# Kernel optimization log

Hardware: AMD Instinct MI355X
Metric: run time of the kernel (lower is better)

The kernel has to match this reference:

```python
import jax, jax.numpy as jnp
import numpy as np


def _cdist(a, b, p):
    # a: [B, N, D], b: [B, M, D] -> [B, N, M] pairwise Lp distance
    diff = jnp.abs(a[:, :, None, :] - b[:, None, :, :])  # [B, N, M, D]
    if p == 1:
        return jnp.sum(diff, axis=-1)
    return jnp.sum(diff ** p, axis=-1) ** (1.0 / p)


def setup_inputs() -> dict:
    key = jax.random.key(0)
    k1, k2, k3 = jax.random.split(key, 3)
    B, P, D = 32, 2048, 2
    pred = jax.random.normal(k1, (B, P, D), dtype=jnp.float32)
    gt = jax.random.normal(k2, (B, P, D), dtype=jnp.float32)
    gt_valid = jax.random.normal(k3, (B, P, D), dtype=jnp.float32)
    return {"pred": pred, "gt": gt, "gt_valid": gt_valid, "loss_type": 1}


def reference(pred, gt, gt_valid, loss_type):
    # matrix = cdist(pred, gt): [B, Np, Ng]; torch.min(dim=1) reduces over Np
    m1 = _cdist(pred, gt, loss_type)
    pred2gt_min = jnp.min(m1, axis=1)  # [B, Ng]
    # matrix = cdist(gt_valid, pred): [B, Ngv, Np]; min over dim=1 (Ngv)
    m2 = _cdist(gt_valid, pred, loss_type)
    gt2pred_min = jnp.min(m2, axis=1)  # [B, Np]
    return jnp.mean(jnp.stack([jnp.mean(pred2gt_min), jnp.mean(gt2pred_min)]))
```

## Files before the change

### kernel.cpp

```cpp
#include <hip/hip_runtime.h>


typedef float v2f __attribute__((ext_vector_type(2)));

#define BB 32
#define NN 2048
#define TPB 512
#define WAVES 8
#define TGT 256
#define CH (NN / WAVES)
#define NTILES (NN / TGT)
#define NBLK (2 * BB * NTILES)

__global__ __launch_bounds__(TPB) void chamfer_l1_part(
    const float* __restrict__ pred,
    const float* __restrict__ gt,
    const float* __restrict__ gt_valid,
    float* __restrict__ bsum)
{
    const int bid  = blockIdx.x;
    const int dir  = bid >> 8;
    const int rem  = bid & 255;
    const int b    = rem >> 3;
    const int tile = rem & (NTILES - 1);
    const int lane = threadIdx.x & 63;
    const int wid  = threadIdx.x >> 6;

    const float* __restrict__ tgt = (dir == 0 ? gt   : pred)     + (size_t)b * NN * 2;
    const float* __restrict__ src = (dir == 0 ? pred : gt_valid) + (size_t)b * NN * 2;

    __shared__ v2f lds_src[NN];
    {
        const float4* gsrc = reinterpret_cast<const float4*>(src);
        float4*       lsrc = reinterpret_cast<float4*>(lds_src);
        lsrc[threadIdx.x]       = gsrc[threadIdx.x];
        lsrc[threadIdx.x + TPB] = gsrc[threadIdx.x + TPB];
    }

    const int j0 = tile * TGT + lane;
    v2f p0, p1, p2, p3;
    {
        float2 t0 = reinterpret_cast<const float2*>(tgt)[j0];
        float2 t1 = reinterpret_cast<const float2*>(tgt)[j0 + 64];
        float2 t2 = reinterpret_cast<const float2*>(tgt)[j0 + 128];
        float2 t3 = reinterpret_cast<const float2*>(tgt)[j0 + 192];
        p0 = (v2f){t0.x, t0.y};
        p1 = (v2f){t1.x, t1.y};
        p2 = (v2f){t2.x, t2.y};
        p3 = (v2f){t3.x, t3.y};
    }
    __syncthreads();

    const float4* __restrict__ ls4 =
        reinterpret_cast<const float4*>(lds_src + (size_t)wid * CH);

    float c00 = 1e30f, c01 = 1e30f, c10 = 1e30f, c11 = 1e30f;
    float c20 = 1e30f, c21 = 1e30f, c30 = 1e30f, c31 = 1e30f;

    #pragma unroll 2
    for (int s = 0; s < CH / 2; s += 4) {
        float4 f0 = ls4[s + 0];
        float4 f1 = ls4[s + 1];
        float4 f2 = ls4[s + 2];
        float4 f3 = ls4[s + 3];
        v2f q0 = (v2f){f0.x, f0.y}, q1 = (v2f){f0.z, f0.w};
        v2f q2 = (v2f){f1.x, f1.y}, q3 = (v2f){f1.z, f1.w};
        v2f q4 = (v2f){f2.x, f2.y}, q5 = (v2f){f2.z, f2.w};
        v2f q6 = (v2f){f3.x, f3.y}, q7 = (v2f){f3.z, f3.w};

        #define L1S(q, p) (fabsf((q).x - (p).x) + fabsf((q).y - (p).y))
        c00 = fminf(c00, fminf(L1S(q0,p0), L1S(q1,p0)));
        c00 = fminf(c00, fminf(L1S(q2,p0), L1S(q3,p0)));
        c01 = fminf(c01, fminf(L1S(q4,p0), L1S(q5,p0)));
        c01 = fminf(c01, fminf(L1S(q6,p0), L1S(q7,p0)));
        c10 = fminf(c10, fminf(L1S(q0,p1), L1S(q1,p1)));
        c10 = fminf(c10, fminf(L1S(q2,p1), L1S(q3,p1)));
        c11 = fminf(c11, fminf(L1S(q4,p1), L1S(q5,p1)));
        c11 = fminf(c11, fminf(L1S(q6,p1), L1S(q7,p1)));
        c20 = fminf(c20, fminf(L1S(q0,p2), L1S(q1,p2)));
        c20 = fminf(c20, fminf(L1S(q2,p2), L1S(q3,p2)));
        c21 = fminf(c21, fminf(L1S(q4,p2), L1S(q5,p2)));
        c21 = fminf(c21, fminf(L1S(q6,p2), L1S(q7,p2)));
        c30 = fminf(c30, fminf(L1S(q0,p3), L1S(q1,p3)));
        c30 = fminf(c30, fminf(L1S(q2,p3), L1S(q3,p3)));
        c31 = fminf(c31, fminf(L1S(q4,p3), L1S(q5,p3)));
        c31 = fminf(c31, fminf(L1S(q6,p3), L1S(q7,p3)));
        #undef L1S
    }
    const float m0 = fminf(c00, c01);
    const float m1 = fminf(c10, c11);
    const float m2 = fminf(c20, c21);
    const float m3 = fminf(c30, c31);

    __shared__ float part[WAVES][TGT];
    part[wid][lane]       = m0;
    part[wid][lane + 64]  = m1;
    part[wid][lane + 128] = m2;
    part[wid][lane + 192] = m3;
    __syncthreads();

    __shared__ float wpart[4];
    if (threadIdx.x < TGT) {
        const int t = threadIdx.x;
        float mm = part[0][t];
        #pragma unroll
        for (int w = 1; w < WAVES; ++w) mm = fminf(mm, part[w][t]);
        for (int off = 32; off > 0; off >>= 1)
            mm += __shfl_down(mm, off, 64);
        if ((t & 63) == 0) wpart[t >> 6] = mm;
    }
    __syncthreads();
    if (threadIdx.x == 0)
        bsum[bid] = (wpart[0] + wpart[1]) + (wpart[2] + wpart[3]);
}

__global__ __launch_bounds__(256) void chamfer_l1_reduce(
    const float* __restrict__ bsum,
    float* __restrict__ out)
{
    const int t = threadIdx.x;
    float2 v = reinterpret_cast<const float2*>(bsum)[t];
    float s = v.x + v.y;
    for (int off = 32; off > 0; off >>= 1)
        s += __shfl_down(s, off, 64);
    __shared__ float w[4];
    if ((t & 63) == 0) w[t >> 6] = s;
    __syncthreads();
    if (t == 0)
        out[0] = (w[0] + w[1] + w[2] + w[3]) * (1.0f / (2.0f * BB * NN));
}

extern "C" void kernel_launch(void* const* d_in, const int* in_sizes, int n_in,
                              void* d_out, int out_size, void* d_ws, size_t ws_size,
                              hipStream_t stream) {
    const float* pred     = (const float*)d_in[0];
    const float* gt       = (const float*)d_in[1];
    const float* gt_valid = (const float*)d_in[2];
    float* out  = (float*)d_out;
    float* bsum = (float*)d_ws;

    chamfer_l1_part<<<NBLK, TPB, 0, stream>>>(pred, gt, gt_valid, bsum);
    chamfer_l1_reduce<<<1, 256, 0, stream>>>(bsum, out);
}
```

Baseline: 82.08 us.

## Rotate points to compute L1 distance as Chebyshev max with packed ops

Uses the identity |dx|+|dy| = max(|du|,|dv|) with u=x+y, v=x-y. Source points are stored pre-rotated in LDS and targets are stored negated, so each pair of distances costs two packed adds, two abs-max ops and one min3 via inline asm. This roughly halves the VALU instruction count per distance in the inner loop. The rotation changes floating-point rounding slightly, and the inline asm limits compiler scheduling.

```diff
diff --git a/kernel.cpp b/kernel.cpp
--- a/kernel.cpp
+++ b/kernel.cpp
@@ -11,6 +11,22 @@
 #define CH (NN / WAVES)
 #define NTILES (NN / TGT)
 #define NBLK (2 * BB * NTILES)
+
+__device__ __forceinline__ v2f pk_add(v2f a, v2f b) {
+    v2f d;
+    asm("v_pk_add_f32 %0, %1, %2" : "=v"(d) : "v"(a), "v"(b));
+    return d;
+}
+__device__ __forceinline__ float max_abs(float a, float b) {
+    float d;
+    asm("v_max_f32 %0, abs(%1), abs(%2)" : "=v"(d) : "v"(a), "v"(b));
+    return d;
+}
+__device__ __forceinline__ float min3(float a, float b, float c) {
+    float d;
+    asm("v_min3_f32 %0, %1, %2, %3" : "=v"(d) : "v"(a), "v"(b), "v"(c));
+    return d;
+}
 
 __global__ __launch_bounds__(TPB) void chamfer_l1_part(
     const float* __restrict__ pred,
@@ -29,33 +45,39 @@
     const float* __restrict__ tgt = (dir == 0 ? gt   : pred)     + (size_t)b * NN * 2;
     const float* __restrict__ src = (dir == 0 ? pred : gt_valid) + (size_t)b * NN * 2;
 
-    __shared__ v2f lds_src[NN];
+    __shared__ float4 lds_src[NN / 2];
     {
         const float4* gsrc = reinterpret_cast<const float4*>(src);
-        float4*       lsrc = reinterpret_cast<float4*>(lds_src);
-        lsrc[threadIdx.x]       = gsrc[threadIdx.x];
-        lsrc[threadIdx.x + TPB] = gsrc[threadIdx.x + TPB];
+        float4 t0 = gsrc[threadIdx.x];
+        float4 t1 = gsrc[threadIdx.x + TPB];
+        lds_src[threadIdx.x]       = (float4){t0.x + t0.y, t0.z + t0.w,
+                                              t0.x - t0.y, t0.z - t0.w};
+        lds_src[threadIdx.x + TPB] = (float4){t1.x + t1.y, t1.z + t1.w,
+                                              t1.x - t1.y, t1.z - t1.w};
     }
 
     const int j0 = tile * TGT + lane;
-    v2f p0, p1, p2, p3;
+    v2f nu0, nv0, nu1, nv1, nu2, nv2, nu3, nv3;
     {
         float2 t0 = reinterpret_cast<const float2*>(tgt)[j0];
         float2 t1 = reinterpret_cast<const float2*>(tgt)[j0 + 64];
         float2 t2 = reinterpret_cast<const float2*>(tgt)[j0 + 128];
         float2 t3 = reinterpret_cast<const float2*>(tgt)[j0 + 192];
-        p0 = (v2f){t0.x, t0.y};
-        p1 = (v2f){t1.x, t1.y};
-        p2 = (v2f){t2.x, t2.y};
-        p3 = (v2f){t3.x, t3.y};
+        nu0 = (v2f){-(t0.x + t0.y), -(t0.x + t0.y)};
+        nv0 = (v2f){-(t0.x - t0.y), -(t0.x - t0.y)};
+        nu1 = (v2f){-(t1.x + t1.y), -(t1.x + t1.y)};
+        nv1 = (v2f){-(t1.x - t1.y), -(t1.x - t1.y)};
+        nu2 = (v2f){-(t2.x + t2.y), -(t2.x + t2.y)};
+        nv2 = (v2f){-(t2.x - t2.y), -(t2.x - t2.y)};
+        nu3 = (v2f){-(t3.x + t3.y), -(t3.x + t3.y)};
+        nv3 = (v2f){-(t3.x - t3.y), -(t3.x - t3.y)};
     }
     __syncthreads();
 
-    const float4* __restrict__ ls4 =
-        reinterpret_cast<const float4*>(lds_src + (size_t)wid * CH);
+    const float4* __restrict__ ls4 = lds_src + (size_t)wid * (CH / 2);
 
-    float c00 = 1e30f, c01 = 1e30f, c10 = 1e30f, c11 = 1e30f;
-    float c20 = 1e30f, c21 = 1e30f, c30 = 1e30f, c31 = 1e30f;
+    float c0A = 1e30f, c0B = 1e30f, c1A = 1e30f, c1B = 1e30f;
+    float c2A = 1e30f, c2B = 1e30f, c3A = 1e30f, c3B = 1e30f;
 
     #pragma unroll 2
     for (int s = 0; s < CH / 2; s += 4) {
@@ -63,34 +85,29 @@
         float4 f1 = ls4[s + 1];
         float4 f2 = ls4[s + 2];
         float4 f3 = ls4[s + 3];
-        v2f q0 = (v2f){f0.x, f0.y}, q1 = (v2f){f0.z, f0.w};
-        v2f q2 = (v2f){f1.x, f1.y}, q3 = (v2f){f1.z, f1.w};
-        v2f q4 = (v2f){f2.x, f2.y}, q5 = (v2f){f2.z, f2.w};
-        v2f q6 = (v2f){f3.x, f3.y}, q7 = (v2f){f3.z, f3.w};
 
-        #define L1S(q, p) (fabsf((q).x - (p).x) + fabsf((q).y - (p).y))
-        c00 = fminf(c00, fminf(L1S(q0,p0), L1S(q1,p0)));
-        c00 = fminf(c00, fminf(L1S(q2,p0), L1S(q3,p0)));
-        c01 = fminf(c01, fminf(L1S(q4,p0), L1S(q5,p0)));
-        c01 = fminf(c01, fminf(L1S(q6,p0), L1S(q7,p0)));
-        c10 = fminf(c10, fminf(L1S(q0,p1), L1S(q1,p1)));
-        c10 = fminf(c10, fminf(L1S(q2,p1), L1S(q3,p1)));
-        c11 = fminf(c11, fminf(L1S(q4,p1), L1S(q5,p1)));
-        c11 = fminf(c11, fminf(L1S(q6,p1), L1S(q7,p1)));
-        c20 = fminf(c20, fminf(L1S(q0,p2), L1S(q1,p2)));
-        c20 = fminf(c20, fminf(L1S(q2,p2), L1S(q3,p2)));
-        c21 = fminf(c21, fminf(L1S(q4,p2), L1S(q5,p2)));
-        c21 = fminf(c21, fminf(L1S(q6,p2), L1S(q7,p2)));
-        c30 = fminf(c30, fminf(L1S(q0,p3), L1S(q1,p3)));
-        c30 = fminf(c30, fminf(L1S(q2,p3), L1S(q3,p3)));
-        c31 = fminf(c31, fminf(L1S(q4,p3), L1S(q5,p3)));
-        c31 = fminf(c31, fminf(L1S(q6,p3), L1S(q7,p3)));
-        #undef L1S
+        #define PAIR2(f, nu, nv, chain)                                   \
+        {                                                                 \
+            v2f du = pk_add((v2f){(f).x, (f).y}, nu);                     \
+            v2f dv = pk_add((v2f){(f).z, (f).w}, nv);                     \
+            float h0 = max_abs(du.x, dv.x);                               \
+            float h1 = max_abs(du.y, dv.y);                               \
+            chain = min3(chain, h0, h1);                                  \
+        }
+        PAIR2(f0, nu0, nv0, c0A) PAIR2(f1, nu0, nv0, c0A)
+        PAIR2(f2, nu0, nv0, c0B) PAIR2(f3, nu0, nv0, c0B)
+        PAIR2(f0, nu1, nv1, c1A) PAIR2(f1, nu1, nv1, c1A)
+        PAIR2(f2, nu1, nv1, c1B) PAIR2(f3, nu1, nv1, c1B)
+        PAIR2(f0, nu2, nv2, c2A) PAIR2(f1, nu2, nv2, c2A)
+        PAIR2(f2, nu2, nv2, c2B) PAIR2(f3, nu2, nv2, c2B)
+        PAIR2(f0, nu3, nv3, c3A) PAIR2(f1, nu3, nv3, c3A)
+        PAIR2(f2, nu3, nv3, c3B) PAIR2(f3, nu3, nv3, c3B)
+        #undef PAIR2
     }
-    const float m0 = fminf(c00, c01);
-    const float m1 = fminf(c10, c11);
-    const float m2 = fminf(c20, c21);
-    const float m3 = fminf(c30, c31);
+    const float m0 = fminf(c0A, c0B);
+    const float m1 = fminf(c1A, c1B);
+    const float m2 = fminf(c2A, c2B);
+    const float m3 = fminf(c3A, c3B);
 
     __shared__ float part[WAVES][TGT];
     part[wid][lane]       = m0;
```

Result: slower. 84.23 us (+2.6%).
